# Kernel tuning notes

Measured on AMD Instinct MI355X. Metric: run time of the kernel, lower is better.

The kernel has to match this reference:

```python
import jax, jax.numpy as jnp
import numpy as np

CHUNK = 32  # chunk_size in _delta_rule_chunkwise

def _l2norm(x, eps=1e-6):
    return x * jax.lax.rsqrt(jnp.sum(x * x, axis=-1, keepdims=True) + eps)

def setup_inputs() -> dict:
    key = jax.random.key(0)
    kq, kk, kv, kb = jax.random.split(key, 4)
    b, h, L, dk, dv = 2, 8, 4096, 128, 128
    return {
        "q": jax.random.normal(kq, (b, h, L, dk), jnp.float32),
        "k": jax.random.normal(kk, (b, h, L, dk), jnp.float32),
        "v": jax.random.normal(kv, (b, h, L, dv), jnp.float32),
        "beta": jax.random.uniform(kb, (b, h, L), jnp.float32),  # sigmoid(b_proj) in (0,1)
    }

def _delta_rule_chunkwise(q, k, v, beta, chunk_size=CHUNK):
    b, h, L, dk = q.shape
    dv = v.shape[-1]
    c = chunk_size
    pad = (-L) % c
    if pad:
        q = jnp.pad(q, ((0, 0), (0, 0), (0, pad), (0, 0)))
        k = jnp.pad(k, ((0, 0), (0, 0), (0, pad), (0, 0)))
        v = jnp.pad(v, ((0, 0), (0, 0), (0, pad), (0, 0)))
        beta = jnp.pad(beta, ((0, 0), (0, 0), (0, pad)))
    n = (L + pad) // c
    q = _l2norm(q)
    k = _l2norm(k)
    v = v * beta[..., None]
    k_beta = k * beta[..., None]
    # [b,h,n,c,d]
    resh = lambda t: t.reshape(b, h, n, c, t.shape[-1])
    q, k, v, k_beta = map(resh, (q, k, v, k_beta))
    # strictly-lower-triangular -(k_beta k^T)
    lower = jnp.tril(jnp.ones((c, c), bool), -1)
    att = -(k_beta @ jnp.swapaxes(k, -1, -2)) * lower
    # forward substitution: invert (I - A) for strictly lower A (unrolled, c=32 static)
    for i in range(1, c):
        upd = jnp.einsum('...j,...jm->...m', att[..., i, :], att[..., :, :i])
        att = att.at[..., i, :i].add(upd)
    att = att + jnp.eye(c, dtype=att.dtype)
    att = att.astype(jnp.bfloat16).astype(q.dtype)  # matches .to(torch.bfloat16)
    u = att @ v         # [b,h,n,c,dv]
    w = att @ k_beta    # [b,h,n,c,dk]
    future = jnp.triu(jnp.ones((c, c), bool), 1)
    S0 = jnp.zeros((b, h, dk, dv), q.dtype)

    def step(S, inp):
        q_i, k_i, u_i, w_i = inp  # [b,h,c,d]
        att_local = jnp.where(future, 0.0, q_i @ jnp.swapaxes(k_i, -1, -2))
        u_new = u_i - w_i @ S
        o_i = q_i @ S + att_local @ u_new
        S_new = S + jnp.swapaxes(k_i, -1, -2) @ u_new
        return S_new, o_i

    xs = tuple(jnp.moveaxis(t, 2, 0) for t in (q, k, u, w))  # scan over chunks
    S, o = jax.lax.scan(step, S0, xs)
    o = jnp.moveaxis(o, 0, 2).reshape(b, h, n * c, dv)[:, :, :L]
    return o, S

def reference(q, k, v, beta):
    return _delta_rule_chunkwise(q, k, v, beta)
```

## Files before the change

### kernel.cpp

```cpp
#include <hip/hip_runtime.h>
#include <hip/hip_bf16.h>


#define B 2
#define H 8
#define LSEQ 4096
#define DK 128
#define DV 128
#define C 32
#define NCHUNK (LSEQ / C)
#define BH (B * H)
#define NBLK (BH * NCHUNK)

typedef _Float16 f16x8 __attribute__((ext_vector_type(8)));
typedef float f32x4 __attribute__((ext_vector_type(4)));

union U4H8 { uint4 u; f16x8 h; };

__device__ inline unsigned short f2h(float f) {
    _Float16 h = (_Float16)f;
    unsigned short u;
    __builtin_memcpy(&u, &h, 2);
    return u;
}
__device__ inline float h2f(unsigned int v) {
    unsigned short s = (unsigned short)v;
    _Float16 h;
    __builtin_memcpy(&h, &s, 2);
    return (float)h;
}
__device__ inline unsigned int pack2(float a, float b) {
    return (unsigned int)f2h(a) | ((unsigned int)f2h(b) << 16);
}
__device__ inline float dot4(float4 a, float4 b) {
    return a.x * b.x + a.y * b.y + a.z * b.z + a.w * b.w;
}

__global__ __launch_bounds__(256, 3) void phase2_kernel(
    const float* __restrict__ q, const float* __restrict__ k,
    const float* __restrict__ v, const float* __restrict__ beta,
    uint4* __restrict__ wnegf, uint4* __restrict__ qnf,
    uint4* __restrict__ ktf, uint4* __restrict__ atf,
    uint2* __restrict__ uf)
{
    __shared__ alignas(16) _Float16 Qh[32 * 136];
    __shared__ alignas(16) _Float16 Kh[32 * 136];
    __shared__ alignas(16) _Float16 VT[128 * 40];
    __shared__ alignas(16) _Float16 KT[128 * 40];
    __shared__ alignas(16) _Float16 Ah[32 * 40];
    __shared__ alignas(16) _Float16 Th[32 * 40];
    __shared__ alignas(16) _Float16 ALh[32 * 40];
    __shared__ float sredQ[256], sredK[256];
    __shared__ float sbeta[32];

    const int t = threadIdx.x;
    const int blk = blockIdx.x;
    const int wv = t >> 6, l = t & 63, lm = l & 15, quad = l >> 4;
    const int r8 = t >> 3, sg = t & 7, c16 = sg * 16;
    const long gbase = ((long)blk * C + r8) * DK + c16;

    float4 qv[4], kv[4], vv[4];
    float sqs = 0.f, sks = 0.f;
    #pragma unroll
    for (int i = 0; i < 4; i++) {
        qv[i] = *(const float4*)(q + gbase + i * 4);
        kv[i] = *(const float4*)(k + gbase + i * 4);
        vv[i] = *(const float4*)(v + gbase + i * 4);
        sqs += dot4(qv[i], qv[i]);
        sks += dot4(kv[i], kv[i]);
    }
    sredQ[r8 * 8 + sg] = sqs;
    sredK[r8 * 8 + sg] = sks;
    if (t < 32) sbeta[t] = beta[(long)blk * C + t];
    __syncthreads();
    float s1 = 0.f, s2 = 0.f;
    #pragma unroll
    for (int j = 0; j < 8; j++) { s1 += sredQ[r8 * 8 + j]; s2 += sredK[r8 * 8 + j]; }
    const float qsc = rsqrtf(s1 + 1e-6f);
    const float ksc = rsqrtf(s2 + 1e-6f);

    {
        uint4 h0, h1;
        h0.x = pack2(qv[0].x * qsc, qv[0].y * qsc); h0.y = pack2(qv[0].z * qsc, qv[0].w * qsc);
        h0.z = pack2(qv[1].x * qsc, qv[1].y * qsc); h0.w = pack2(qv[1].z * qsc, qv[1].w * qsc);
        h1.x = pack2(qv[2].x * qsc, qv[2].y * qsc); h1.y = pack2(qv[2].z * qsc, qv[2].w * qsc);
        h1.z = pack2(qv[3].x * qsc, qv[3].y * qsc); h1.w = pack2(qv[3].z * qsc, qv[3].w * qsc);
        *(uint4*)&Qh[r8 * 136 + c16] = h0;
        *(uint4*)&Qh[r8 * 136 + c16 + 8] = h1;
        uint4 g0, g1;
        g0.x = pack2(kv[0].x * ksc, kv[0].y * ksc); g0.y = pack2(kv[0].z * ksc, kv[0].w * ksc);
        g0.z = pack2(kv[1].x * ksc, kv[1].y * ksc); g0.w = pack2(kv[1].z * ksc, kv[1].w * ksc);
        g1.x = pack2(kv[2].x * ksc, kv[2].y * ksc); g1.y = pack2(kv[2].z * ksc, kv[2].w * ksc);
        g1.z = pack2(kv[3].x * ksc, kv[3].y * ksc); g1.w = pack2(kv[3].z * ksc, kv[3].w * ksc);
        *(uint4*)&Kh[r8 * 136 + c16] = g0;
        *(uint4*)&Kh[r8 * 136 + c16 + 8] = g1;
        const float* vf = (const float*)vv;
        const float* kf = (const float*)kv;
        #pragma unroll
        for (int i = 0; i < 16; i++) {
            VT[(c16 + i) * 40 + r8] = (_Float16)vf[i];
            KT[(c16 + i) * 40 + r8] = (_Float16)(kf[i] * ksc);
        }
    }
    __syncthreads();

    const int mi = wv >> 1, ni = wv & 1;
    const int colx = ni * 16 + lm;

    {
        f32x4 cAtt = {0.f, 0.f, 0.f, 0.f}, cAl = {0.f, 0.f, 0.f, 0.f};
        #pragma unroll
        for (int kt = 0; kt < 4; kt++) {
            U4H8 ka, qa, kb;
            ka.u = *(const uint4*)&Kh[(mi * 16 + lm) * 136 + kt * 32 + quad * 8];
            qa.u = *(const uint4*)&Qh[(mi * 16 + lm) * 136 + kt * 32 + quad * 8];
            kb.u = *(const uint4*)&Kh[(ni * 16 + lm) * 136 + kt * 32 + quad * 8];
            cAtt = __builtin_amdgcn_mfma_f32_16x16x32_f16(ka.h, kb.h, cAtt, 0, 0, 0);
            cAl  = __builtin_amdgcn_mfma_f32_16x16x32_f16(qa.h, kb.h, cAl, 0, 0, 0);
        }
        float4 brow = *(const float4*)&sbeta[mi * 16 + quad * 4];
        float br[4] = {brow.x, brow.y, brow.z, brow.w};
        #pragma unroll
        for (int r = 0; r < 4; r++) {
            int row = mi * 16 + quad * 4 + r;
            float av = (colx < row) ? (-br[r] * cAtt[r]) : 0.f;
            Ah[row * 40 + colx] = (_Float16)av;
            Th[row * 40 + colx] = (_Float16)((colx == row) ? 1.0f : av);
            ALh[row * 40 + colx] = (_Float16)((colx <= row) ? cAl[r] : 0.f);
        }
    }
    __syncthreads();

    #pragma unroll
    for (int i = 0; i < 2; i++) {
        int slot = t + i * 256;
        int f = slot >> 6, ln = slot & 63, flm = ln & 15, fq = ln >> 4;
        int mt2 = f >> 2, kt = f & 3;
        qnf[((long)blk * 8 + f) * 64 + ln] =
            *(const uint4*)&Qh[(mt2 * 16 + flm) * 136 + kt * 32 + fq * 8];
        ktf[((long)blk * 8 + f) * 64 + ln] =
            *(const uint4*)&KT[(f * 16 + flm) * 40 + fq * 8];
    }
    if (t < 128) {
        int f = t >> 6, ln = t & 63, flm = ln & 15, fq = ln >> 4;
        atf[((long)blk * 2 + f) * 64 + ln] =
            *(const uint4*)&ALh[(f * 16 + flm) * 40 + fq * 8];
    }

    #pragma unroll 1
    for (int p = 0; p < 4; p++) {
        U4H8 aA, bA;
        aA.u = *(const uint4*)&Ah[(mi * 16 + lm) * 40 + quad * 8];
        #pragma unroll
        for (int j = 0; j < 8; j++) bA.h[j] = Ah[(quad * 8 + j) * 40 + colx];
        f32x4 cA = {0.f, 0.f, 0.f, 0.f};
        cA = __builtin_amdgcn_mfma_f32_16x16x32_f16(aA.h, bA.h, cA, 0, 0, 0);
        __syncthreads();
        #pragma unroll
        for (int r = 0; r < 4; r++)
            Ah[(mi * 16 + quad * 4 + r) * 40 + colx] = (_Float16)cA[r];
        __syncthreads();
        U4H8 aA2, bT;
        aA2.u = *(const uint4*)&Ah[(mi * 16 + lm) * 40 + quad * 8];
        #pragma unroll
        for (int j = 0; j < 8; j++) bT.h[j] = Th[(quad * 8 + j) * 40 + colx];
        f32x4 cT;
        #pragma unroll
        for (int r = 0; r < 4; r++)
            cT[r] = (float)Th[(mi * 16 + quad * 4 + r) * 40 + colx];
        cT = __builtin_amdgcn_mfma_f32_16x16x32_f16(aA2.h, bT.h, cT, 0, 0, 0);
        __syncthreads();
        #pragma unroll
        for (int r = 0; r < 4; r++)
            Th[(mi * 16 + quad * 4 + r) * 40 + colx] = (_Float16)cT[r];
        __syncthreads();
    }

    {
        int c4 = (t & 7) * 4;
        #pragma unroll
        for (int i = 0; i < 4; i++) {
            int cth = c4 + i;
            float tvv = (float)Th[r8 * 40 + cth];
            tvv = __bfloat162float(__float2bfloat16(tvv));
            Ah[r8 * 40 + cth] = (_Float16)(tvv * sbeta[cth]);
        }
    }
    __syncthreads();

    {
        U4H8 aT[2];
        aT[0].u = *(const uint4*)&Ah[(0 * 16 + lm) * 40 + quad * 8];
        aT[1].u = *(const uint4*)&Ah[(1 * 16 + lm) * 40 + quad * 8];
        #pragma unroll
        for (int e = 0; e < 2; e++) {
            int ntt = wv * 2 + e;
            U4H8 bV, bK;
            bV.u = *(const uint4*)&VT[(ntt * 16 + lm) * 40 + quad * 8];
            bK.u = *(const uint4*)&KT[(ntt * 16 + lm) * 40 + quad * 8];
            #pragma unroll
            for (int mt2 = 0; mt2 < 2; mt2++) {
                f32x4 z = {0.f, 0.f, 0.f, 0.f};
                f32x4 cU = __builtin_amdgcn_mfma_f32_16x16x32_f16(aT[mt2].h, bV.h, z, 0, 0, 0);
                f32x4 cW = __builtin_amdgcn_mfma_f32_16x16x32_f16(aT[mt2].h, bK.h, z, 0, 0, 0);
                uint2 ou;
                ou.x = pack2(cU[0], cU[1]); ou.y = pack2(cU[2], cU[3]);
                uf[(((long)blk * 2 + mt2) * 8 + ntt) * 64 + l] = ou;
                #pragma unroll
                for (int r = 0; r < 4; r++)
                    Qh[(mt2 * 16 + quad * 4 + r) * 136 + ntt * 16 + lm] = (_Float16)(-cW[r]);
            }
        }
    }
    __syncthreads();
    #pragma unroll
    for (int i = 0; i < 2; i++) {
        int slot = t + i * 256;
        int f = slot >> 6, ln = slot & 63, flm = ln & 15, fq = ln >> 4;
        int mt2 = f >> 2, kt = f & 3;
        wnegf[((long)blk * 8 + f) * 64 + ln] =
            *(const uint4*)&Qh[(mt2 * 16 + flm) * 136 + kt * 32 + fq * 8];
    }
}

struct Frags {
    uint4 aW[2][4];
    uint4 aQ[2][4];
    uint4 aK[8];
    uint4 aAt[2];
    uint2 aU[2];
};

__global__ __launch_bounds__(64, 1) void phase3_kernel(
    const uint4* __restrict__ wnegf, const uint4* __restrict__ qnf,
    const uint4* __restrict__ ktf, const uint4* __restrict__ atf,
    const uint2* __restrict__ uf,
    float* __restrict__ o_out, float* __restrict__ S_out)
{
    __shared__ alignas(16) _Float16 S16[16 * 136];
    __shared__ alignas(16) _Float16 U16[16 * 40];

    const int l = threadIdx.x;
    const int lm = l & 15, quad = l >> 4, dvl = lm & 7;
    const int bh = blockIdx.x & 15;
    const int w = blockIdx.x >> 4;
    const int dv = w * 16 + lm;

    f32x4 accS[8];
    #pragma unroll
    for (int mt = 0; mt < 8; mt++) accS[mt] = (f32x4){0.f, 0.f, 0.f, 0.f};

    auto loadf = [&](Frags& f, int nc) {
        long blk = (long)bh * NCHUNK + nc;
        #pragma unroll
        for (int mt2 = 0; mt2 < 2; mt2++) {
            #pragma unroll
            for (int kt = 0; kt < 4; kt++) {
                f.aW[mt2][kt] = wnegf[(blk * 8 + mt2 * 4 + kt) * 64 + l];
                f.aQ[mt2][kt] = qnf[(blk * 8 + mt2 * 4 + kt) * 64 + l];
            }
            f.aAt[mt2] = atf[(blk * 2 + mt2) * 64 + l];
            f.aU[mt2] = uf[((blk * 2 + mt2) * 8 + w) * 64 + l];
        }
        #pragma unroll
        for (int mt = 0; mt < 8; mt++) f.aK[mt] = ktf[(blk * 8 + mt) * 64 + l];
    };

    auto compute = [&](const Frags& f, int nc) {
        #pragma unroll
        for (int mt = 0; mt < 8; mt++) {
            int dk0 = mt * 16 + quad * 4;
            int phys = (dk0 >> 3) ^ dvl;
            int sub = dk0 & 7;
            uint2 p;
            p.x = pack2(accS[mt][0], accS[mt][1]);
            p.y = pack2(accS[mt][2], accS[mt][3]);
            *(uint2*)&S16[lm * 136 + phys * 8 + sub] = p;
        }
        __builtin_amdgcn_sched_barrier(0);
        f32x4 accU[2], accO[2];
        #pragma unroll
        for (int mt2 = 0; mt2 < 2; mt2++) {
            accU[mt2][0] = h2f(f.aU[mt2].x & 0xffffu);
            accU[mt2][1] = h2f(f.aU[mt2].x >> 16);
            accU[mt2][2] = h2f(f.aU[mt2].y & 0xffffu);
            accU[mt2][3] = h2f(f.aU[mt2].y >> 16);
            accO[mt2] = (f32x4){0.f, 0.f, 0.f, 0.f};
        }
        #pragma unroll
        for (int kt = 0; kt < 4; kt++) {
            int phys = (kt * 4 + quad) ^ dvl;
            U4H8 bs;
            bs.u = *(const uint4*)&S16[lm * 136 + phys * 8];
            #pragma unroll
            for (int mt2 = 0; mt2 < 2; mt2++) {
                U4H8 aw, aq;
                aw.u = f.aW[mt2][kt];
                aq.u = f.aQ[mt2][kt];
                accU[mt2] = __builtin_amdgcn_mfma_f32_16x16x32_f16(aw.h, bs.h, accU[mt2], 0, 0, 0);
                accO[mt2] = __builtin_amdgcn_mfma_f32_16x16x32_f16(aq.h, bs.h, accO[mt2], 0, 0, 0);
            }
        }
        #pragma unroll
        for (int mt2 = 0; mt2 < 2; mt2++) {
            int s0 = mt2 * 16 + quad * 4;
            uint2 p;
            p.x = pack2(accU[mt2][0], accU[mt2][1]);
            p.y = pack2(accU[mt2][2], accU[mt2][3]);
            *(uint2*)&U16[lm * 40 + s0] = p;
        }
        __builtin_amdgcn_sched_barrier(0);
        U4H8 bu;
        bu.u = *(const uint4*)&U16[lm * 40 + quad * 8];
        const long ob = ((long)bh * LSEQ + (long)nc * C) * DV;
        #pragma unroll
        for (int mt2 = 0; mt2 < 2; mt2++) {
            U4H8 aa;
            aa.u = f.aAt[mt2];
            accO[mt2] = __builtin_amdgcn_mfma_f32_16x16x32_f16(aa.h, bu.h, accO[mt2], 0, 0, 0);
            #pragma unroll
            for (int r = 0; r < 4; r++)
                o_out[ob + (long)(mt2 * 16 + quad * 4 + r) * DV + dv] = accO[mt2][r];
        }
        #pragma unroll
        for (int mt = 0; mt < 8; mt++) {
            U4H8 ak;
            ak.u = f.aK[mt];
            accS[mt] = __builtin_amdgcn_mfma_f32_16x16x32_f16(ak.h, bu.h, accS[mt], 0, 0, 0);
        }
    };

    Frags fA, fB;
    loadf(fA, 0);
    #pragma unroll 1
    for (int nc = 0; nc < NCHUNK; nc += 2) {
        loadf(fB, (nc + 1 < NCHUNK - 1) ? nc + 1 : NCHUNK - 1);
        compute(fA, nc);
        loadf(fA, (nc + 2 < NCHUNK - 1) ? nc + 2 : NCHUNK - 1);
        compute(fB, nc + 1);
    }
    #pragma unroll
    for (int mt = 0; mt < 8; mt++) {
        #pragma unroll
        for (int r = 0; r < 4; r++)
            S_out[(long)bh * (DK * DV) + (long)(mt * 16 + quad * 4 + r) * DV + dv] = accS[mt][r];
    }
}

extern "C" void kernel_launch(void* const* d_in, const int* in_sizes, int n_in,
                              void* d_out, int out_size, void* d_ws, size_t ws_size,
                              hipStream_t stream) {
    const float* q    = (const float*)d_in[0];
    const float* k    = (const float*)d_in[1];
    const float* v    = (const float*)d_in[2];
    const float* beta = (const float*)d_in[3];

    float* o = (float*)d_out;
    float* S = o + (long)BH * LSEQ * DV;

    const size_t nwq = (size_t)NBLK * 8 * 64;
    uint4* wnegf = (uint4*)d_ws;
    uint4* qnf = wnegf + nwq;
    uint4* ktf = qnf + nwq;
    uint4* atf = ktf + nwq;
    uint2* uf  = (uint2*)(atf + (size_t)NBLK * 2 * 64);

    phase2_kernel<<<NBLK, 256, 0, stream>>>(q, k, v, beta, wnegf, qnf, ktf, atf, uf);
    phase3_kernel<<<BH * 8, 64, 0, stream>>>(wnegf, qnf, ktf, atf, uf, o, S);
}
```

Measured before the change: 250.1 us.

## Rewrite per-chunk prep kernel as single-wave register-resident MFMA pipeline

The per-chunk preparation kernel now runs one 64-lane wave per chunk instead of four waves. Q/K fragments are loaded straight into MFMA register layout, with L2 norms reduced by shuffles and the normalization scale applied after the Gram matmuls. The triangular inverse is built by a doubling scheme that keeps the A and T blocks plus their transposes, so no __syncthreads barriers are needed. The scan kernel's LDS staging for S and U switches from XOR swizzling to a grouped 8-wide layout and drops the sched_barriers. The risk is much less parallelism per block and strided uncoalesced global reads for V and K in the final stage.

```diff
diff --git a/kernel.cpp b/kernel.cpp
--- a/kernel.cpp
+++ b/kernel.cpp
@@ -35,191 +35,303 @@
 __device__ inline float dot4(float4 a, float4 b) {
     return a.x * b.x + a.y * b.y + a.z * b.z + a.w * b.w;
 }
-
-__global__ __launch_bounds__(256, 3) void phase2_kernel(
-    const float* __restrict__ q, const float* __restrict__ k,
-    const float* __restrict__ v, const float* __restrict__ beta,
+__device__ inline float bf16r(float x) {
+    return __bfloat162float(__float2bfloat16(x));
+}
+__device__ inline uint2 pk4(float v0, float v1, float v2, float v3) {
+    uint2 p; p.x = pack2(v0, v1); p.y = pack2(v2, v3); return p;
+}
+
+#define S40 40
+#define S136 136
+
+__global__ __launch_bounds__(64) void phase2_kernel(
+    const float* __restrict__ qg, const float* __restrict__ kg,
+    const float* __restrict__ vg, const float* __restrict__ betag,
     uint4* __restrict__ wnegf, uint4* __restrict__ qnf,
     uint4* __restrict__ ktf, uint4* __restrict__ atf,
     uint2* __restrict__ uf)
 {
-    __shared__ alignas(16) _Float16 Qh[32 * 136];
-    __shared__ alignas(16) _Float16 Kh[32 * 136];
-    __shared__ alignas(16) _Float16 VT[128 * 40];
-    __shared__ alignas(16) _Float16 KT[128 * 40];
-    __shared__ alignas(16) _Float16 Ah[32 * 40];
-    __shared__ alignas(16) _Float16 Th[32 * 40];
-    __shared__ alignas(16) _Float16 ALh[32 * 40];
-    __shared__ float sredQ[256], sredK[256];
-    __shared__ float sbeta[32];
-
-    const int t = threadIdx.x;
+    __shared__ alignas(16) _Float16 sA [32 * S40];
+    __shared__ alignas(16) _Float16 sAT[32 * S40];
+    __shared__ alignas(16) _Float16 sTT[32 * S40];
+    __shared__ alignas(16) _Float16 sTB[32 * S40];
+    __shared__ alignas(16) _Float16 sW [32 * S136];
+    __shared__ alignas(16) float sbetaL[32];
+    __shared__ alignas(16) float skscL[32];
+
+    const int l = threadIdx.x;
+    const int lm = l & 15, qd = l >> 4;
     const int blk = blockIdx.x;
-    const int wv = t >> 6, l = t & 63, lm = l & 15, quad = l >> 4;
-    const int r8 = t >> 3, sg = t & 7, c16 = sg * 16;
-    const long gbase = ((long)blk * C + r8) * DK + c16;
-
-    float4 qv[4], kv[4], vv[4];
-    float sqs = 0.f, sks = 0.f;
-    #pragma unroll
-    for (int i = 0; i < 4; i++) {
-        qv[i] = *(const float4*)(q + gbase + i * 4);
-        kv[i] = *(const float4*)(k + gbase + i * 4);
-        vv[i] = *(const float4*)(v + gbase + i * 4);
-        sqs += dot4(qv[i], qv[i]);
-        sks += dot4(kv[i], kv[i]);
-    }
-    sredQ[r8 * 8 + sg] = sqs;
-    sredK[r8 * 8 + sg] = sks;
-    if (t < 32) sbeta[t] = beta[(long)blk * C + t];
-    __syncthreads();
-    float s1 = 0.f, s2 = 0.f;
-    #pragma unroll
-    for (int j = 0; j < 8; j++) { s1 += sredQ[r8 * 8 + j]; s2 += sredK[r8 * 8 + j]; }
-    const float qsc = rsqrtf(s1 + 1e-6f);
-    const float ksc = rsqrtf(s2 + 1e-6f);
+    const long tb = (long)blk * C * DK;
+    const f32x4 z4 = {0.f, 0.f, 0.f, 0.f};
+
+    if (l < 32) sbetaL[l] = betag[(long)blk * C + l];
+
+    U4H8 qF[8], kF[8];
+    float ssq[2] = {0.f, 0.f}, ssk[2] = {0.f, 0.f};
+    #pragma unroll
+    for (int mt = 0; mt < 2; mt++) {
+        #pragma unroll
+        for (int kt = 0; kt < 4; kt++) {
+            const float* qp = qg + tb + (long)(mt * 16 + lm) * DK + kt * 32 + qd * 8;
+            const float* kp = kg + tb + (long)(mt * 16 + lm) * DK + kt * 32 + qd * 8;
+            float4 a0 = *(const float4*)qp, a1 = *(const float4*)(qp + 4);
+            float4 b0 = *(const float4*)kp, b1 = *(const float4*)(kp + 4);
+            ssq[mt] += dot4(a0, a0) + dot4(a1, a1);
+            ssk[mt] += dot4(b0, b0) + dot4(b1, b1);
+            U4H8 x;
+            x.u.x = pack2(a0.x, a0.y); x.u.y = pack2(a0.z, a0.w);
+            x.u.z = pack2(a1.x, a1.y); x.u.w = pack2(a1.z, a1.w);
+            qF[mt * 4 + kt] = x;
+            U4H8 y;
+            y.u.x = pack2(b0.x, b0.y); y.u.y = pack2(b0.z, b0.w);
+            y.u.z = pack2(b1.x, b1.y); y.u.w = pack2(b1.z, b1.w);
+            kF[mt * 4 + kt] = y;
+        }
+    }
+    float qsc[2], ksc[2];
+    #pragma unroll
+    for (int mt = 0; mt < 2; mt++) {
+        float s = ssq[mt];
+        s += __shfl_xor(s, 16, 64);
+        s += __shfl_xor(s, 32, 64);
+        qsc[mt] = rsqrtf(s + 1e-6f);
+        float t = ssk[mt];
+        t += __shfl_xor(t, 16, 64);
+        t += __shfl_xor(t, 32, 64);
+        ksc[mt] = rsqrtf(t + 1e-6f);
+    }
+    if (qd == 0) { skscL[lm] = ksc[0]; skscL[16 + lm] = ksc[1]; }
+
+    f32x4 alT[3] = {z4, z4, z4};
+    #pragma unroll
+    for (int kt = 0; kt < 4; kt++) {
+        alT[0] = __builtin_amdgcn_mfma_f32_16x16x32_f16(kF[kt].h,     qF[kt].h,     alT[0], 0, 0, 0);
+        alT[1] = __builtin_amdgcn_mfma_f32_16x16x32_f16(kF[kt].h,     qF[4 + kt].h, alT[1], 0, 0, 0);
+        alT[2] = __builtin_amdgcn_mfma_f32_16x16x32_f16(kF[4 + kt].h, qF[4 + kt].h, alT[2], 0, 0, 0);
+    }
+    #pragma unroll
+    for (int mt = 0; mt < 2; mt++) {
+        _Float16 qs = (_Float16)qsc[mt];
+        #pragma unroll
+        for (int kt = 0; kt < 4; kt++) {
+            U4H8 x;
+            x.h = qF[mt * 4 + kt].h * qs;
+            qnf[((long)blk * 8 + mt * 4 + kt) * 64 + l] = x.u;
+        }
+    }
+    f32x4 rw[4] = {z4, z4, z4, z4};
+    #pragma unroll
+    for (int kt = 0; kt < 4; kt++) {
+        rw[0] = __builtin_amdgcn_mfma_f32_16x16x32_f16(kF[kt].h,     kF[kt].h,     rw[0], 0, 0, 0);
+        rw[1] = __builtin_amdgcn_mfma_f32_16x16x32_f16(kF[kt].h,     kF[4 + kt].h, rw[1], 0, 0, 0);
+        rw[2] = __builtin_amdgcn_mfma_f32_16x16x32_f16(kF[4 + kt].h, kF[kt].h,     rw[2], 0, 0, 0);
+        rw[3] = __builtin_amdgcn_mfma_f32_16x16x32_f16(kF[4 + kt].h, kF[4 + kt].h, rw[3], 0, 0, 0);
+    }
+
+    float4 b4[2], ks4[2];
+    b4[0]  = *(const float4*)&sbetaL[qd * 4];      b4[1]  = *(const float4*)&sbetaL[16 + qd * 4];
+    ks4[0] = *(const float4*)&skscL[qd * 4];       ks4[1] = *(const float4*)&skscL[16 + qd * 4];
+    const float bcol0 = sbetaL[lm], bcol1 = sbetaL[16 + lm];
+    const float bA4[2] = {(&b4[0].x)[0], 0.f}; (void)bA4;
 
     {
-        uint4 h0, h1;
-        h0.x = pack2(qv[0].x * qsc, qv[0].y * qsc); h0.y = pack2(qv[0].z * qsc, qv[0].w * qsc);
-        h0.z = pack2(qv[1].x * qsc, qv[1].y * qsc); h0.w = pack2(qv[1].z * qsc, qv[1].w * qsc);
-        h1.x = pack2(qv[2].x * qsc, qv[2].y * qsc); h1.y = pack2(qv[2].z * qsc, qv[2].w * qsc);
-        h1.z = pack2(qv[3].x * qsc, qv[3].y * qsc); h1.w = pack2(qv[3].z * qsc, qv[3].w * qsc);
-        *(uint4*)&Qh[r8 * 136 + c16] = h0;
-        *(uint4*)&Qh[r8 * 136 + c16 + 8] = h1;
-        uint4 g0, g1;
-        g0.x = pack2(kv[0].x * ksc, kv[0].y * ksc); g0.y = pack2(kv[0].z * ksc, kv[0].w * ksc);
-        g0.z = pack2(kv[1].x * ksc, kv[1].y * ksc); g0.w = pack2(kv[1].z * ksc, kv[1].w * ksc);
-        g1.x = pack2(kv[2].x * ksc, kv[2].y * ksc); g1.y = pack2(kv[2].z * ksc, kv[2].w * ksc);
-        g1.z = pack2(kv[3].x * ksc, kv[3].y * ksc); g1.w = pack2(kv[3].z * ksc, kv[3].w * ksc);
-        *(uint4*)&Kh[r8 * 136 + c16] = g0;
-        *(uint4*)&Kh[r8 * 136 + c16 + 8] = g1;
-        const float* vf = (const float*)vv;
-        const float* kf = (const float*)kv;
-        #pragma unroll
-        for (int i = 0; i < 16; i++) {
-            VT[(c16 + i) * 40 + r8] = (_Float16)vf[i];
-            KT[(c16 + i) * 40 + r8] = (_Float16)(kf[i] * ksc);
-        }
-    }
-    __syncthreads();
-
-    const int mi = wv >> 1, ni = wv & 1;
-    const int colx = ni * 16 + lm;
+        *(uint2*)&sTB[lm * S40 + 16 + qd * 4] = (uint2){0u, 0u};
+        float v[4];
+        #pragma unroll
+        for (int r = 0; r < 4; r++) {
+            int c = qd * 4 + r;
+            v[r] = (c <= lm) ? (qsc[0] * (&ks4[0].x)[r] * alT[0][r]) : 0.f;
+        }
+        *(uint2*)&sTB[lm * S40 + qd * 4] = pk4(v[0], v[1], v[2], v[3]);
+        #pragma unroll
+        for (int r = 0; r < 4; r++) v[r] = qsc[1] * (&ks4[0].x)[r] * alT[1][r];
+        *(uint2*)&sTB[(16 + lm) * S40 + qd * 4] = pk4(v[0], v[1], v[2], v[3]);
+        #pragma unroll
+        for (int r = 0; r < 4; r++) {
+            int c = qd * 4 + r;
+            v[r] = (c <= lm) ? (qsc[1] * (&ks4[1].x)[r] * alT[2][r]) : 0.f;
+        }
+        *(uint2*)&sTB[(16 + lm) * S40 + 16 + qd * 4] = pk4(v[0], v[1], v[2], v[3]);
+    }
+    #pragma unroll
+    for (int f = 0; f < 2; f++) {
+        uint4 x = *(const uint4*)&sTB[(f * 16 + lm) * S40 + qd * 8];
+        atf[((long)blk * 2 + f) * 64 + l] = x;
+    }
 
     {
-        f32x4 cAtt = {0.f, 0.f, 0.f, 0.f}, cAl = {0.f, 0.f, 0.f, 0.f};
+        float v[4];
+        *(uint2*)&sA [lm * S40 + 16 + qd * 4]        = (uint2){0u, 0u};
+        *(uint2*)&sAT[(16 + lm) * S40 + qd * 4]      = (uint2){0u, 0u};
+        *(uint2*)&sTT[(16 + lm) * S40 + qd * 4]      = (uint2){0u, 0u};
+        #pragma unroll
+        for (int r = 0; r < 4; r++) {
+            int c = qd * 4 + r;
+            v[r] = (c < lm) ? (-bcol0 * ksc[0] * (&ks4[0].x)[r] * rw[0][r]) : 0.f;
+        }
+        *(uint2*)&sA[lm * S40 + qd * 4] = pk4(v[0], v[1], v[2], v[3]);
+        #pragma unroll
+        for (int r = 0; r < 4; r++) v[r] = -bcol1 * ksc[1] * (&ks4[0].x)[r] * rw[1][r];
+        *(uint2*)&sA[(16 + lm) * S40 + qd * 4] = pk4(v[0], v[1], v[2], v[3]);
+        #pragma unroll
+        for (int r = 0; r < 4; r++) {
+            int c = qd * 4 + r;
+            v[r] = (c < lm) ? (-bcol1 * ksc[1] * (&ks4[1].x)[r] * rw[3][r]) : 0.f;
+        }
+        *(uint2*)&sA[(16 + lm) * S40 + 16 + qd * 4] = pk4(v[0], v[1], v[2], v[3]);
+        #pragma unroll
+        for (int r = 0; r < 4; r++) {
+            int c = qd * 4 + r;
+            v[r] = (c > lm) ? (-(&b4[0].x)[r] * (&ks4[0].x)[r] * ksc[0] * rw[0][r]) : 0.f;
+        }
+        *(uint2*)&sAT[lm * S40 + qd * 4] = pk4(v[0], v[1], v[2], v[3]);
+        #pragma unroll
+        for (int r = 0; r < 4; r++) v[r] = -(&b4[1].x)[r] * (&ks4[1].x)[r] * ksc[0] * rw[2][r];
+        *(uint2*)&sAT[lm * S40 + 16 + qd * 4] = pk4(v[0], v[1], v[2], v[3]);
+        #pragma unroll
+        for (int r = 0; r < 4; r++) {
+            int c = qd * 4 + r;
+            v[r] = (c > lm) ? (-(&b4[1].x)[r] * (&ks4[1].x)[r] * ksc[1] * rw[3][r]) : 0.f;
+        }
+        *(uint2*)&sAT[(16 + lm) * S40 + 16 + qd * 4] = pk4(v[0], v[1], v[2], v[3]);
+        #pragma unroll
+        for (int r = 0; r < 4; r++) {
+            int c = qd * 4 + r;
+            v[r] = (c > lm) ? (-(&b4[0].x)[r] * (&ks4[0].x)[r] * ksc[0] * rw[0][r])
+                            : ((c == lm) ? 1.0f : 0.f);
+        }
+        *(uint2*)&sTT[lm * S40 + qd * 4] = pk4(v[0], v[1], v[2], v[3]);
+        #pragma unroll
+        for (int r = 0; r < 4; r++) v[r] = -(&b4[1].x)[r] * (&ks4[1].x)[r] * ksc[0] * rw[2][r];
+        *(uint2*)&sTT[lm * S40 + 16 + qd * 4] = pk4(v[0], v[1], v[2], v[3]);
+        #pragma unroll
+        for (int r = 0; r < 4; r++) {
+            int c = qd * 4 + r;
+            v[r] = (c > lm) ? (-(&b4[1].x)[r] * (&ks4[1].x)[r] * ksc[1] * rw[3][r])
+                            : ((c == lm) ? 1.0f : 0.f);
+        }
+        *(uint2*)&sTT[(16 + lm) * S40 + 16 + qd * 4] = pk4(v[0], v[1], v[2], v[3]);
+    }
+    f32x4 Tc[3], TTc[3];
+    #pragma unroll
+    for (int r = 0; r < 4; r++) {
+        int rr = qd * 4 + r;
+        Tc[0][r] = (lm < rr) ? (-(&b4[0].x)[r] * (&ks4[0].x)[r] * ksc[0] * rw[0][r])
+                             : ((lm == rr) ? 1.0f : 0.f);
+        Tc[1][r] = -(&b4[1].x)[r] * (&ks4[1].x)[r] * ksc[0] * rw[2][r];
+        Tc[2][r] = (lm < rr) ? (-(&b4[1].x)[r] * (&ks4[1].x)[r] * ksc[1] * rw[3][r])
+                             : ((lm == rr) ? 1.0f : 0.f);
+        TTc[0][r] = (rr < lm) ? (-bcol0 * ksc[0] * (&ks4[0].x)[r] * rw[0][r])
+                              : ((rr == lm) ? 1.0f : 0.f);
+        TTc[1][r] = -bcol1 * ksc[1] * (&ks4[0].x)[r] * rw[1][r];
+        TTc[2][r] = (rr < lm) ? (-bcol1 * ksc[1] * (&ks4[1].x)[r] * rw[3][r])
+                              : ((rr == lm) ? 1.0f : 0.f);
+    }
+
+    #pragma unroll
+    for (int p = 0; p < 4; p++) {
+        U4H8 AF[2], ATF[2], TTF[2];
+        AF[0].u  = *(const uint4*)&sA [lm * S40 + qd * 8];
+        AF[1].u  = *(const uint4*)&sA [(16 + lm) * S40 + qd * 8];
+        ATF[0].u = *(const uint4*)&sAT[lm * S40 + qd * 8];
+        ATF[1].u = *(const uint4*)&sAT[(16 + lm) * S40 + qd * 8];
+        TTF[0].u = *(const uint4*)&sTT[lm * S40 + qd * 8];
+        TTF[1].u = *(const uint4*)&sTT[(16 + lm) * S40 + qd * 8];
+
+        f32x4 A2_00 = __builtin_amdgcn_mfma_f32_16x16x32_f16(AF[0].h, ATF[0].h, z4, 0, 0, 0);
+        f32x4 A2_10 = __builtin_amdgcn_mfma_f32_16x16x32_f16(AF[1].h, ATF[0].h, z4, 0, 0, 0);
+        f32x4 A2_11 = __builtin_amdgcn_mfma_f32_16x16x32_f16(AF[1].h, ATF[1].h, z4, 0, 0, 0);
+        f32x4 A2T_00 = __builtin_amdgcn_mfma_f32_16x16x32_f16(ATF[0].h, AF[0].h, z4, 0, 0, 0);
+        f32x4 A2T_01 = __builtin_amdgcn_mfma_f32_16x16x32_f16(ATF[0].h, AF[1].h, z4, 0, 0, 0);
+        f32x4 A2T_11 = __builtin_amdgcn_mfma_f32_16x16x32_f16(ATF[1].h, AF[1].h, z4, 0, 0, 0);
+
+        {
+            float v[4];
+            #pragma unroll
+            for (int r = 0; r < 4; r++) { int c = qd * 4 + r; v[r] = (c < lm) ? A2T_00[r] : 0.f; }
+            *(uint2*)&sA[lm * S40 + qd * 4] = pk4(v[0], v[1], v[2], v[3]);
+            *(uint2*)&sA[(16 + lm) * S40 + qd * 4] = pk4(A2T_01[0], A2T_01[1], A2T_01[2], A2T_01[3]);
+            #pragma unroll
+            for (int r = 0; r < 4; r++) { int c = qd * 4 + r; v[r] = (c < lm) ? A2T_11[r] : 0.f; }
+            *(uint2*)&sA[(16 + lm) * S40 + 16 + qd * 4] = pk4(v[0], v[1], v[2], v[3]);
+        }
+        if (p < 3) {
+            float v[4];
+            #pragma unroll
+            for (int r = 0; r < 4; r++) { int c = qd * 4 + r; v[r] = (c > lm) ? A2_00[r] : 0.f; }
+            *(uint2*)&sAT[lm * S40 + qd * 4] = pk4(v[0], v[1], v[2], v[3]);
+            *(uint2*)&sAT[lm * S40 + 16 + qd * 4] = pk4(A2_10[0], A2_10[1], A2_10[2], A2_10[3]);
+            #pragma unroll
+            for (int r = 0; r < 4; r++) { int c = qd * 4 + r; v[r] = (c > lm) ? A2_11[r] : 0.f; }
+            *(uint2*)&sAT[(16 + lm) * S40 + 16 + qd * 4] = pk4(v[0], v[1], v[2], v[3]);
+        }
+        U4H8 AnF[2];
+        AnF[0].u = *(const uint4*)&sA[lm * S40 + qd * 8];
+        AnF[1].u = *(const uint4*)&sA[(16 + lm) * S40 + qd * 8];
+        Tc[0]  = __builtin_amdgcn_mfma_f32_16x16x32_f16(AnF[0].h, TTF[0].h, Tc[0], 0, 0, 0);
+        Tc[1]  = __builtin_amdgcn_mfma_f32_16x16x32_f16(AnF[1].h, TTF[0].h, Tc[1], 0, 0, 0);
+        Tc[2]  = __builtin_amdgcn_mfma_f32_16x16x32_f16(AnF[1].h, TTF[1].h, Tc[2], 0, 0, 0);
+        TTc[0] = __builtin_amdgcn_mfma_f32_16x16x32_f16(TTF[0].h, AnF[0].h, TTc[0], 0, 0, 0);
+        TTc[1] = __builtin_amdgcn_mfma_f32_16x16x32_f16(TTF[0].h, AnF[1].h, TTc[1], 0, 0, 0);
+        TTc[2] = __builtin_amdgcn_mfma_f32_16x16x32_f16(TTF[1].h, AnF[1].h, TTc[2], 0, 0, 0);
+        if (p < 3) {
+            *(uint2*)&sTT[lm * S40 + qd * 4]             = pk4(Tc[0][0], Tc[0][1], Tc[0][2], Tc[0][3]);
+            *(uint2*)&sTT[lm * S40 + 16 + qd * 4]        = pk4(Tc[1][0], Tc[1][1], Tc[1][2], Tc[1][3]);
+            *(uint2*)&sTT[(16 + lm) * S40 + 16 + qd * 4] = pk4(Tc[2][0], Tc[2][1], Tc[2][2], Tc[2][3]);
+        }
+    }
+
+    {
+        *(uint2*)&sTB[lm * S40 + 16 + qd * 4] = (uint2){0u, 0u};
+        float v[4];
+        #pragma unroll
+        for (int r = 0; r < 4; r++) v[r] = bf16r(TTc[0][r]) * (&b4[0].x)[r];
+        *(uint2*)&sTB[lm * S40 + qd * 4] = pk4(v[0], v[1], v[2], v[3]);
+        #pragma unroll
+        for (int r = 0; r < 4; r++) v[r] = bf16r(TTc[1][r]) * (&b4[0].x)[r];
+        *(uint2*)&sTB[(16 + lm) * S40 + qd * 4] = pk4(v[0], v[1], v[2], v[3]);
+        #pragma unroll
+        for (int r = 0; r < 4; r++) v[r] = bf16r(TTc[2][r]) * (&b4[1].x)[r];
+        *(uint2*)&sTB[(16 + lm) * S40 + 16 + qd * 4] = pk4(v[0], v[1], v[2], v[3]);
+    }
+    U4H8 TbF[2];
+    TbF[0].u = *(const uint4*)&sTB[lm * S40 + qd * 8];
+    TbF[1].u = *(const uint4*)&sTB[(16 + lm) * S40 + qd * 8];
+
+    float kscj[8];
+    #pragma unroll
+    for (int j = 0; j < 8; j++) kscj[j] = skscL[qd * 8 + j];
+    #pragma unroll
+    for (int nt = 0; nt < 8; nt++) {
+        U4H8 bV, bK;
+        #pragma unroll
+        for (int j = 0; j < 8; j++) {
+            const long ro = tb + (long)(qd * 8 + j) * DK + nt * 16 + lm;
+            bV.h[j] = (_Float16)vg[ro];
+            bK.h[j] = (_Float16)(kg[ro] * kscj[j]);
+        }
+        ktf[((long)blk * 8 + nt) * 64 + l] = bK.u;
+        f32x4 u0 = __builtin_amdgcn_mfma_f32_16x16x32_f16(TbF[0].h, bV.h, z4, 0, 0, 0);
+        f32x4 u1 = __builtin_amdgcn_mfma_f32_16x16x32_f16(TbF[1].h, bV.h, z4, 0, 0, 0);
+        uf[(((long)blk * 2 + 0) * 8 + nt) * 64 + l] = pk4(u0[0], u0[1], u0[2], u0[3]);
+        uf[(((long)blk * 2 + 1) * 8 + nt) * 64 + l] = pk4(u1[0], u1[1], u1[2], u1[3]);
+        f32x4 w0 = __builtin_amdgcn_mfma_f32_16x16x32_f16(TbF[0].h, bK.h, z4, 0, 0, 0);
+        f32x4 w1 = __builtin_amdgcn_mfma_f32_16x16x32_f16(TbF[1].h, bK.h, z4, 0, 0, 0);
+        #pragma unroll
+        for (int r = 0; r < 4; r++) {
+            sW[(qd * 4 + r) * S136 + nt * 16 + lm]        = (_Float16)(-w0[r]);
+            sW[(16 + qd * 4 + r) * S136 + nt * 16 + lm]   = (_Float16)(-w1[r]);
+        }
+    }
+    #pragma unroll
+    for (int mt2 = 0; mt2 < 2; mt2++) {
         #pragma unroll
         for (int kt = 0; kt < 4; kt++) {
-            U4H8 ka, qa, kb;
-            ka.u = *(const uint4*)&Kh[(mi * 16 + lm) * 136 + kt * 32 + quad * 8];
-            qa.u = *(const uint4*)&Qh[(mi * 16 + lm) * 136 + kt * 32 + quad * 8];
-            kb.u = *(const uint4*)&Kh[(ni * 16 + lm) * 136 + kt * 32 + quad * 8];
-            cAtt = __builtin_amdgcn_mfma_f32_16x16x32_f16(ka.h, kb.h, cAtt, 0, 0, 0);
-            cAl  = __builtin_amdgcn_mfma_f32_16x16x32_f16(qa.h, kb.h, cAl, 0, 0, 0);
-        }
-        float4 brow = *(const float4*)&sbeta[mi * 16 + quad * 4];
-        float br[4] = {brow.x, brow.y, brow.z, brow.w};
-        #pragma unroll
-        for (int r = 0; r < 4; r++) {
-            int row = mi * 16 + quad * 4 + r;
-            float av = (colx < row) ? (-br[r] * cAtt[r]) : 0.f;
-            Ah[row * 40 + colx] = (_Float16)av;
-            Th[row * 40 + colx] = (_Float16)((colx == row) ? 1.0f : av);
-            ALh[row * 40 + colx] = (_Float16)((colx <= row) ? cAl[r] : 0.f);
-        }
-    }
-    __syncthreads();
-
-    #pragma unroll
-    for (int i = 0; i < 2; i++) {
-        int slot = t + i * 256;
-        int f = slot >> 6, ln = slot & 63, flm = ln & 15, fq = ln >> 4;
-        int mt2 = f >> 2, kt = f & 3;
-        qnf[((long)blk * 8 + f) * 64 + ln] =
-            *(const uint4*)&Qh[(mt2 * 16 + flm) * 136 + kt * 32 + fq * 8];
-        ktf[((long)blk * 8 + f) * 64 + ln] =
-            *(const uint4*)&KT[(f * 16 + flm) * 40 + fq * 8];
-    }
-    if (t < 128) {
-        int f = t >> 6, ln = t & 63, flm = ln & 15, fq = ln >> 4;
-        atf[((long)blk * 2 + f) * 64 + ln] =
-            *(const uint4*)&ALh[(f * 16 + flm) * 40 + fq * 8];
-    }
-
-    #pragma unroll 1
-    for (int p = 0; p < 4; p++) {
-        U4H8 aA, bA;
-        aA.u = *(const uint4*)&Ah[(mi * 16 + lm) * 40 + quad * 8];
-        #pragma unroll
-        for (int j = 0; j < 8; j++) bA.h[j] = Ah[(quad * 8 + j) * 40 + colx];
-        f32x4 cA = {0.f, 0.f, 0.f, 0.f};
-        cA = __builtin_amdgcn_mfma_f32_16x16x32_f16(aA.h, bA.h, cA, 0, 0, 0);
-        __syncthreads();
-        #pragma unroll
-        for (int r = 0; r < 4; r++)
-            Ah[(mi * 16 + quad * 4 + r) * 40 + colx] = (_Float16)cA[r];
-        __syncthreads();
-        U4H8 aA2, bT;
-        aA2.u = *(const uint4*)&Ah[(mi * 16 + lm) * 40 + quad * 8];
-        #pragma unroll
-        for (int j = 0; j < 8; j++) bT.h[j] = Th[(quad * 8 + j) * 40 + colx];
-        f32x4 cT;
-        #pragma unroll
-        for (int r = 0; r < 4; r++)
-            cT[r] = (float)Th[(mi * 16 + quad * 4 + r) * 40 + colx];
-        cT = __builtin_amdgcn_mfma_f32_16x16x32_f16(aA2.h, bT.h, cT, 0, 0, 0);
-        __syncthreads();
-        #pragma unroll
-        for (int r = 0; r < 4; r++)
-            Th[(mi * 16 + quad * 4 + r) * 40 + colx] = (_Float16)cT[r];
-        __syncthreads();
-    }
-
-    {
-        int c4 = (t & 7) * 4;
-        #pragma unroll
-        for (int i = 0; i < 4; i++) {
-            int cth = c4 + i;
-            float tvv = (float)Th[r8 * 40 + cth];
-            tvv = __bfloat162float(__float2bfloat16(tvv));
-            Ah[r8 * 40 + cth] = (_Float16)(tvv * sbeta[cth]);
-        }
-    }
-    __syncthreads();
-
-    {
-        U4H8 aT[2];
-        aT[0].u = *(const uint4*)&Ah[(0 * 16 + lm) * 40 + quad * 8];
-        aT[1].u = *(const uint4*)&Ah[(1 * 16 + lm) * 40 + quad * 8];
-        #pragma unroll
-        for (int e = 0; e < 2; e++) {
-            int ntt = wv * 2 + e;
-            U4H8 bV, bK;
-            bV.u = *(const uint4*)&VT[(ntt * 16 + lm) * 40 + quad * 8];
-            bK.u = *(const uint4*)&KT[(ntt * 16 + lm) * 40 + quad * 8];
-            #pragma unroll
-            for (int mt2 = 0; mt2 < 2; mt2++) {
-                f32x4 z = {0.f, 0.f, 0.f, 0.f};
-                f32x4 cU = __builtin_amdgcn_mfma_f32_16x16x32_f16(aT[mt2].h, bV.h, z, 0, 0, 0);
-                f32x4 cW = __builtin_amdgcn_mfma_f32_16x16x32_f16(aT[mt2].h, bK.h, z, 0, 0, 0);
-                uint2 ou;
-                ou.x = pack2(cU[0], cU[1]); ou.y = pack2(cU[2], cU[3]);
-                uf[(((long)blk * 2 + mt2) * 8 + ntt) * 64 + l] = ou;
-                #pragma unroll
-                for (int r = 0; r < 4; r++)
-                    Qh[(mt2 * 16 + quad * 4 + r) * 136 + ntt * 16 + lm] = (_Float16)(-cW[r]);
-            }
-        }
-    }
-    __syncthreads();
-    #pragma unroll
-    for (int i = 0; i < 2; i++) {
-        int slot = t + i * 256;
-        int f = slot >> 6, ln = slot & 63, flm = ln & 15, fq = ln >> 4;
-        int mt2 = f >> 2, kt = f & 3;
-        wnegf[((long)blk * 8 + f) * 64 + ln] =
-            *(const uint4*)&Qh[(mt2 * 16 + flm) * 136 + kt * 32 + fq * 8];
+            uint4 x = *(const uint4*)&sW[(mt2 * 16 + lm) * S136 + kt * 32 + qd * 8];
+            wnegf[((long)blk * 8 + mt2 * 4 + kt) * 64 + l] = x;
+        }
     }
 }
 
@@ -237,11 +349,11 @@
     const uint2* __restrict__ uf,
     float* __restrict__ o_out, float* __restrict__ S_out)
 {
-    __shared__ alignas(16) _Float16 S16[16 * 136];
-    __shared__ alignas(16) _Float16 U16[16 * 40];
+    __shared__ alignas(16) _Float16 S16[16 * 16 * 8];
+    __shared__ alignas(16) _Float16 U16[4 * 16 * 8];
 
     const int l = threadIdx.x;
-    const int lm = l & 15, quad = l >> 4, dvl = lm & 7;
+    const int lm = l & 15, quad = l >> 4;
     const int bh = blockIdx.x & 15;
     const int w = blockIdx.x >> 4;
     const int dv = w * 16 + lm;
@@ -269,15 +381,11 @@
     auto compute = [&](const Frags& f, int nc) {
         #pragma unroll
         for (int mt = 0; mt < 8; mt++) {
-            int dk0 = mt * 16 + quad * 4;
-            int phys = (dk0 >> 3) ^ dvl;
-            int sub = dk0 & 7;
-            uint2 p;
-            p.x = pack2(accS[mt][0], accS[mt][1]);
-            p.y = pack2(accS[mt][2], accS[mt][3]);
-            *(uint2*)&S16[lm * 136 + phys * 8 + sub] = p;
-        }
-        __builtin_amdgcn_sched_barrier(0);
+            int g = 2 * mt + (quad >> 1);
+            int sub = (quad & 1) * 4;
+            *(uint2*)&S16[(g * 16 + lm) * 8 + sub] =
+                pk4(accS[mt][0], accS[mt][1], accS[mt][2], accS[mt][3]);
+        }
         f32x4 accU[2], accO[2];
         #pragma unroll
         for (int mt2 = 0; mt2 < 2; mt2++) {
@@ -289,9 +397,8 @@
         }
         #pragma unroll
         for (int kt = 0; kt < 4; kt++) {
-            int phys = (kt * 4 + quad) ^ dvl;
             U4H8 bs;
-            bs.u = *(const uint4*)&S16[lm * 136 + phys * 8];
+            bs.u = *(const uint4*)&S16[((kt * 4 + quad) * 16 + lm) * 8];
             #pragma unroll
             for (int mt2 = 0; mt2 < 2; mt2++) {
                 U4H8 aw, aq;
@@ -303,15 +410,13 @@
         }
         #pragma unroll
         for (int mt2 = 0; mt2 < 2; mt2++) {
-            int s0 = mt2 * 16 + quad * 4;
-            uint2 p;
-            p.x = pack2(accU[mt2][0], accU[mt2][1]);
-            p.y = pack2(accU[mt2][2], accU[mt2][3]);
-            *(uint2*)&U16[lm * 40 + s0] = p;
-        }
-        __builtin_amdgcn_sched_barrier(0);
+            int g = 2 * mt2 + (quad >> 1);
+            int sub = (quad & 1) * 4;
+            *(uint2*)&U16[(g * 16 + lm) * 8 + sub] =
+                pk4(accU[mt2][0], accU[mt2][1], accU[mt2][2], accU[mt2][3]);
+        }
         U4H8 bu;
-        bu.u = *(const uint4*)&U16[lm * 40 + quad * 8];
+        bu.u = *(const uint4*)&U16[(quad * 16 + lm) * 8];
         const long ob = ((long)bh * LSEQ + (long)nc * C) * DV;
         #pragma unroll
         for (int mt2 = 0; mt2 < 2; mt2++) {
@@ -365,6 +470,6 @@
     uint4* atf = ktf + nwq;
     uint2* uf  = (uint2*)(atf + (size_t)NBLK * 2 * 64);
 
-    phase2_kernel<<<NBLK, 256, 0, stream>>>(q, k, v, beta, wnegf, qnf, ktf, atf, uf);
+    phase2_kernel<<<NBLK, 64, 0, stream>>>(q, k, v, beta, wnegf, qnf, ktf, atf, uf);
     phase3_kernel<<<BH * 8, 64, 0, stream>>>(wnegf, qnf, ktf, atf, uf, o, S);
 }
```

Result: faster. 233.2 us (-6.7%).
